# Performance work log

Hardware: AMD Instinct MI355X
Metric: run time of the kernel (lower is better)

The kernel has to match this reference:

```python
import jax, jax.numpy as jnp
import numpy as np

B, T, D_IN, D_H, D_CODE, N_CODES, D_OUT = 64, 512, 1024, 512, 256, 128, 100


def setup_inputs() -> dict:
    key = jax.random.key(0)
    ks = jax.random.split(key, 8)
    x = jax.random.normal(ks[0], (B, T, D_IN), dtype=jnp.float32)
    W1 = jax.random.normal(ks[1], (D_IN, D_H), dtype=jnp.float32) * (1.0 / np.sqrt(D_IN))
    b1 = jnp.zeros((D_H,), jnp.float32)
    W2 = jax.random.normal(ks[2], (D_H, D_CODE), dtype=jnp.float32) * (1.0 / np.sqrt(D_H))
    b2 = jnp.zeros((D_CODE,), jnp.float32)
    codebook = jax.random.normal(ks[3], (N_CODES, D_CODE), dtype=jnp.float32)
    Wd = jax.random.normal(ks[4], (D_CODE, D_OUT), dtype=jnp.float32) * (1.0 / np.sqrt(D_CODE))
    bd = jnp.zeros((D_OUT,), jnp.float32)
    return {"x": x, "W1": W1, "b1": b1, "W2": W2, "b2": b2,
            "codebook": codebook, "Wd": Wd, "bd": bd}


def reference(x, W1, b1, W2, b2, codebook, Wd, bd):
    Bb, Tt, _ = x.shape
    # Encoder (per-timestep loop in torch == one batched matmul)
    h = jax.nn.relu(jnp.einsum('btd,dh->bth', x, W1) + b1)
    encoded = jnp.einsum('bth,hc->btc', h, W2) + b2          # [B,T,256]
    flat = encoded.reshape(-1, D_CODE)                        # [B*T,256]
    # Squared euclidean distances (argmin identical to cdist argmin)
    d2 = (jnp.sum(flat * flat, axis=1, keepdims=True)
          - 2.0 * flat @ codebook.T
          + jnp.sum(codebook * codebook, axis=1))             # [B*T,128]
    token_indices = jnp.argmin(d2, axis=-1)                   # [B*T]
    quantized = codebook[token_indices].reshape(Bb, Tt, D_CODE)
    commitment_loss = jnp.mean((encoded - jax.lax.stop_gradient(quantized)) ** 2)
    codebook_loss = jnp.mean((quantized - jax.lax.stop_gradient(encoded)) ** 2)
    # decoded is computed in the torch model but never returned (dead code)
    pooled = encoded.mean(axis=1)
    decoded = pooled @ Wd + bd  # noqa: F841 (pruned by XLA, kept for fidelity)
    total_loss = commitment_loss + 0.25 * codebook_loss
    return (token_indices.reshape(Bb, Tt), commitment_loss, codebook_loss, total_loss)
```

## Files before the change

### kernel.cpp

```cpp
#include <hip/hip_runtime.h>
#include <cstddef>
#include <cstdint>

static constexpr int M_ROWS  = 32768;
static constexpr int D_INK   = 1024;
static constexpr int D_HID   = 512;
static constexpr int D_CODE_ = 256;
static constexpr int N_CODES_= 128;

static constexpr float TAU_GAP = 0.20f;

using f16x8 = __attribute__((ext_vector_type(8))) _Float16;
using f32x4 = __attribute__((ext_vector_type(4))) float;


__device__ __forceinline__ void dma16(const void* g, void* l) {
    __builtin_amdgcn_global_load_lds(
        (const __attribute__((address_space(1))) void*)g,
        (__attribute__((address_space(3))) void*)l, 16, 0, 0);
}

__device__ __forceinline__ void stage_panel(const _Float16* __restrict__ p,
                                            _Float16* dst, int w, int lane)
{
    #pragma unroll
    for (int ii = 0; ii < 2; ++ii) {
        const int I = 2 * w + ii;
        dma16(p + (size_t)I * 512 + lane * 8, dst + (size_t)I * 512);
    }
}

__device__ __forceinline__ void mfma_tile(const _Float16* sA, const _Float16* sB,
                                          int wm, int wn, int kq, int lm,
                                          f32x4 (&acc)[4][4])
{
    f16x8 a[4];
    #pragma unroll
    for (int fm = 0; fm < 4; ++fm)
        a[fm] = *(const f16x8*)(sA + (kq * 128 + wm * 64 + fm * 16 + lm) * 8);
    #pragma unroll
    for (int fn = 0; fn < 4; ++fn) {
        const f16x8 b = *(const f16x8*)(sB + (kq * 128 + wn * 64 + fn * 16 + lm) * 8);
        #pragma unroll
        for (int fm = 0; fm < 4; ++fm)
            acc[fm][fn] = __builtin_amdgcn_mfma_f32_16x16x32_f16(a[fm], b, acc[fm][fn], 0, 0, 0);
    }
}

__device__ __forceinline__ int xcd_swz(int bid, int nwg) {
    const int q = nwg >> 3;
    return (bid & 7) * q + (bid >> 3);
}

__global__ __launch_bounds__(256)
void prep_cb_kernel(const float* __restrict__ cb, _Float16* __restrict__ cbP,
                    float* __restrict__ cbnorm, float* __restrict__ accum,
                    int* __restrict__ cnt)
{
    const int j = blockIdx.x;
    const int t = threadIdx.x;
    const float v = cb[j * D_CODE_ + t];
    const int ks = t >> 5, kq = (t >> 3) & 3, jj = t & 7;
    cbP[((size_t)ks * 512 + kq * 128 + j) * 8 + jj] = (_Float16)v;

    __shared__ float sr[256];
    sr[t] = v * v;
    __syncthreads();
    for (int s = 128; s >= 1; s >>= 1) {
        if (t < s) sr[t] += sr[t + s];
        __syncthreads();
    }
    if (t == 0) cbnorm[j] = sr[0];
    if (j == 0 && t < 2) accum[t] = 0.0f;
    if (j == 0 && t == 2) *cnt = 0;
}

__global__ __launch_bounds__(256)
void pack_w_kernel(const float* __restrict__ W, _Float16* __restrict__ WP,
                   int Kd, int Nd)
{
    const int ks = blockIdx.x, nt = blockIdx.y;
    const int t = threadIdx.x;
    _Float16* dst = WP + ((size_t)nt * (Kd >> 5) + ks) * 4096;
    #pragma unroll
    for (int half = 0; half < 2; ++half) {
        const int f = half * 256 + t;
        const int nc = f & 127, kq = f >> 7;
        f16x8 v;
        #pragma unroll
        for (int j = 0; j < 8; ++j)
            v[j] = (_Float16)W[(size_t)(ks * 32 + kq * 8 + j) * Nd + nt * 128 + nc];
        *(f16x8*)(dst + (size_t)f * 8) = v;
    }
}

__global__ __launch_bounds__(256)
void pack_x_kernel(const float* __restrict__ X, _Float16* __restrict__ XP)
{
    __shared__ _Float16 sh[128][136];
    const int t  = threadIdx.x;
    const int mt = blockIdx.x;
    const int kc = blockIdx.y;

    const float* src = X + (size_t)mt * 128 * D_INK + kc * 128;
    #pragma unroll
    for (int i = 0; i < 16; ++i) {
        const int idx = i * 256 + t;
        const int row = idx >> 5, c4 = idx & 31;
        const float4 v = *(const float4*)(src + (size_t)row * D_INK + c4 * 4);
        _Float16* d = &sh[row][c4 * 4];
        d[0] = (_Float16)v.x; d[1] = (_Float16)v.y;
        d[2] = (_Float16)v.z; d[3] = (_Float16)v.w;
    }
    __syncthreads();

    _Float16* dst = XP + ((size_t)mt * 32 + kc * 4) * 4096;
    #pragma unroll
    for (int s = 0; s < 4; ++s) {
        #pragma unroll
        for (int half = 0; half < 2; ++half) {
            const int f = half * 256 + t;
            const int rc = f & 127, kq = f >> 7;
            const f16x8 v = *(const f16x8*)(&sh[rc][s * 32 + kq * 8]);
            *(f16x8*)(dst + (size_t)s * 4096 + (size_t)f * 8) = v;
        }
    }
}

__global__ __launch_bounds__(256, 4)
void gemm1_kernel(const _Float16* __restrict__ AP, const _Float16* __restrict__ BP,
                  const float* __restrict__ bias, _Float16* __restrict__ CP)
{
    __shared__ _Float16 lds[2][2][4096];

    const int tid  = threadIdx.x;
    const int lane = tid & 63;
    const int w    = tid >> 6;
    const int wm = w >> 1, wn = w & 1;
    const int kq = lane >> 4, lm = lane & 15;

    const int swz = xcd_swz(blockIdx.x, (M_ROWS / 128) * (D_HID / 128));
    const int n0 = (swz & 3) * 128;
    const int m0 = (swz >> 2) * 128;

    const _Float16* Apan = AP + ((size_t)(m0 >> 7) * 32) * 4096;
    const _Float16* Bpan = BP + ((size_t)(n0 >> 7) * 32) * 4096;

    f32x4 acc[4][4] = {};

    stage_panel(Apan, &lds[0][0][0], w, lane);
    stage_panel(Bpan, &lds[0][1][0], w, lane);

    constexpr int NSTEP = D_INK / 32;
    for (int t = 0; t < NSTEP; ++t) {
        const int cur = t & 1, nxt = cur ^ 1;
        __syncthreads();
        if (t + 1 < NSTEP) {
            stage_panel(Apan + (size_t)(t + 1) * 4096, &lds[nxt][0][0], w, lane);
            stage_panel(Bpan + (size_t)(t + 1) * 4096, &lds[nxt][1][0], w, lane);
        }
        mfma_tile(&lds[cur][0][0], &lds[cur][1][0], wm, wn, kq, lm, acc);
    }

    #pragma unroll
    for (int fn = 0; fn < 4; ++fn) {
        const int col = n0 + wn * 64 + fn * 16 + lm;
        const float bv = bias[col];
        #pragma unroll
        for (int fm = 0; fm < 4; ++fm) {
            #pragma unroll
            for (int r = 0; r < 4; ++r) {
                const int row = m0 + wm * 64 + fm * 16 + kq * 4 + r;
                const float v = fmaxf(acc[fm][fn][r] + bv, 0.0f);
                CP[(((size_t)(row >> 7) * 16 + (col >> 5)) * 512
                    + (size_t)((col >> 3) & 3) * 128 + (row & 127)) * 8 + (col & 7)]
                    = (_Float16)v;
            }
        }
    }
}

__global__ __launch_bounds__(256, 4)
void gemm2_kernel(const _Float16* __restrict__ AP, const _Float16* __restrict__ BP,
                  const float* __restrict__ bias, _Float16* __restrict__ CP,
                  float* __restrict__ accum)
{
    __shared__ _Float16 lds[2][2][4096];

    const int tid  = threadIdx.x;
    const int lane = tid & 63;
    const int w    = tid >> 6;
    const int wm = w >> 1, wn = w & 1;
    const int kq = lane >> 4, lm = lane & 15;

    const int swz = xcd_swz(blockIdx.x, (M_ROWS / 128) * (D_CODE_ / 128));
    const int n0 = (swz & 1) * 128;
    const int m0 = (swz >> 1) * 128;

    const _Float16* Apan = AP + ((size_t)(m0 >> 7) * 16) * 4096;
    const _Float16* Bpan = BP + ((size_t)(n0 >> 7) * 16) * 4096;

    f32x4 acc[4][4] = {};

    stage_panel(Apan, &lds[0][0][0], w, lane);
    stage_panel(Bpan, &lds[0][1][0], w, lane);

    constexpr int NSTEP = D_HID / 32;
    for (int t = 0; t < NSTEP; ++t) {
        const int cur = t & 1, nxt = cur ^ 1;
        __syncthreads();
        if (t + 1 < NSTEP) {
            stage_panel(Apan + (size_t)(t + 1) * 4096, &lds[nxt][0][0], w, lane);
            stage_panel(Bpan + (size_t)(t + 1) * 4096, &lds[nxt][1][0], w, lane);
        }
        mfma_tile(&lds[cur][0][0], &lds[cur][1][0], wm, wn, kq, lm, acc);
    }

    float sumsq = 0.0f;
    #pragma unroll
    for (int fn = 0; fn < 4; ++fn) {
        const int col = n0 + wn * 64 + fn * 16 + lm;
        const float bv = bias[col];
        #pragma unroll
        for (int fm = 0; fm < 4; ++fm) {
            #pragma unroll
            for (int r = 0; r < 4; ++r) {
                const int row = m0 + wm * 64 + fm * 16 + kq * 4 + r;
                const float v = acc[fm][fn][r] + bv;
                sumsq = fmaf(v, v, sumsq);
                CP[(((size_t)(row >> 7) * 8 + (col >> 5)) * 512
                    + (size_t)((col >> 3) & 3) * 128 + (row & 127)) * 8 + (col & 7)]
                    = (_Float16)v;
            }
        }
    }
    #pragma unroll
    for (int mk = 1; mk <= 32; mk <<= 1) sumsq += __shfl_xor(sumsq, mk);
    if (lane == 0) atomicAdd(&accum[1], sumsq);
}

__global__ __launch_bounds__(256, 4)
void dist_kernel(const _Float16* __restrict__ AP, const _Float16* __restrict__ BP,
                 const float* __restrict__ cbn,
                 float* __restrict__ outIdx, float* __restrict__ accum,
                 int* __restrict__ cnt, int* __restrict__ list)
{
    __shared__ _Float16 lds[2][2][4096];

    const int tid  = threadIdx.x;
    const int lane = tid & 63;
    const int w    = tid >> 6;
    const int wm = w >> 1, wn = w & 1;
    const int kq = lane >> 4, lm = lane & 15;
    const int m0 = blockIdx.x * 128;

    float cbn_l[4];
    #pragma unroll
    for (int fn = 0; fn < 4; ++fn) cbn_l[fn] = cbn[wn * 64 + fn * 16 + lm];

    const _Float16* Apan = AP + ((size_t)(m0 >> 7) * 8) * 4096;

    f32x4 acc[4][4] = {};

    stage_panel(Apan, &lds[0][0][0], w, lane);
    stage_panel(BP,   &lds[0][1][0], w, lane);

    constexpr int NSTEP = D_CODE_ / 32;
    for (int t = 0; t < NSTEP; ++t) {
        const int cur = t & 1, nxt = cur ^ 1;
        __syncthreads();
        if (t + 1 < NSTEP) {
            stage_panel(Apan + (size_t)(t + 1) * 4096, &lds[nxt][0][0], w, lane);
            stage_panel(BP   + (size_t)(t + 1) * 4096, &lds[nxt][1][0], w, lane);
        }
        mfma_tile(&lds[cur][0][0], &lds[cur][1][0], wm, wn, kq, lm, acc);
    }

    __syncthreads();
    float* eb1 = (float*)&lds[0][0][0];
    float* eb2 = eb1 + 256;
    int*   eix = (int*)(eb2 + 256);

    #pragma unroll
    for (int fm = 0; fm < 4; ++fm) {
        #pragma unroll
        for (int r = 0; r < 4; ++r) {
            float b1v = 3.4e38f, b2v = 3.4e38f; int bi = 0;
            #pragma unroll
            for (int fn = 0; fn < 4; ++fn) {
                const float v = fmaf(-2.0f, acc[fm][fn][r], cbn_l[fn]);
                if (v < b1v) { b2v = b1v; b1v = v; bi = wn * 64 + fn * 16 + lm; }
                else if (v < b2v) b2v = v;
            }
            #pragma unroll
            for (int mk = 1; mk <= 8; mk <<= 1) {
                const float o1 = __shfl_xor(b1v, mk);
                const float o2 = __shfl_xor(b2v, mk);
                const int   oi = __shfl_xor(bi,  mk);
                if (o1 < b1v || (o1 == b1v && oi < bi)) { b2v = fminf(b1v, o2); b1v = o1; bi = oi; }
                else b2v = fminf(b2v, o1);
            }
            const int rl = wm * 64 + fm * 16 + kq * 4 + r;
            if (lm == 0) { eb1[wn * 128 + rl] = b1v; eb2[wn * 128 + rl] = b2v; eix[wn * 128 + rl] = bi; }
        }
    }
    __syncthreads();

    if (tid < 128) {
        const int rl = tid;
        const float a1 = eb1[rl], a2 = eb2[rl]; const int ai = eix[rl];
        const float o1 = eb1[128 + rl], o2 = eb2[128 + rl]; const int oi = eix[128 + rl];
        float B1, B2; int BI;
        if (o1 < a1 || (o1 == a1 && oi < ai)) { B1 = o1; BI = oi; B2 = fminf(a1, o2); }
        else                                  { B1 = a1; BI = ai; B2 = fminf(a2, o1); }
        outIdx[m0 + rl] = (float)BI;
        if (B2 - B1 < TAU_GAP) { const int p = atomicAdd(cnt, 1); list[p] = m0 + rl; }
        float s = B1;
        #pragma unroll
        for (int mk = 1; mk <= 32; mk <<= 1) s += __shfl_xor(s, mk);
        if (lane == 0) atomicAdd(&accum[0], s);
    }
}

__global__ __launch_bounds__(256)
void fixup_kernel(const float* __restrict__ x, const float* __restrict__ W1,
                  const float* __restrict__ b1, const float* __restrict__ W2,
                  const float* __restrict__ b2, const float* __restrict__ cb,
                  const float* __restrict__ cbnorm,
                  const int* __restrict__ cnt, const int* __restrict__ list,
                  float* __restrict__ outIdx)
{
    __shared__ float xr[1024];
    __shared__ float hr[512];
    __shared__ float er[256];
    __shared__ float dv[128];
    __shared__ int   di[128];

    const int tid = threadIdx.x;
    const int n = *cnt;
    for (int it = blockIdx.x; it < n; it += gridDim.x) {
        const int row = list[it];
        __syncthreads();
        #pragma unroll
        for (int i = 0; i < 4; ++i)
            xr[tid + i * 256] = x[(size_t)row * D_INK + tid + i * 256];
        __syncthreads();
        {
            const int c = tid * 2;
            float s0a = 0.f, s0b = 0.f, s1a = 0.f, s1b = 0.f;
            #pragma unroll 4
            for (int k = 0; k < D_INK; k += 2) {
                const float xv0 = xr[k], xv1 = xr[k + 1];
                const float2 w0 = *(const float2*)(W1 + (size_t)k * D_HID + c);
                const float2 w1 = *(const float2*)(W1 + (size_t)(k + 1) * D_HID + c);
                s0a = fmaf(xv0, w0.x, s0a); s1a = fmaf(xv0, w0.y, s1a);
                s0b = fmaf(xv1, w1.x, s0b); s1b = fmaf(xv1, w1.y, s1b);
            }
            hr[c]     = fmaxf(s0a + s0b + b1[c], 0.f);
            hr[c + 1] = fmaxf(s1a + s1b + b1[c + 1], 0.f);
        }
        __syncthreads();
        {
            float sa = 0.f, sb = 0.f;
            #pragma unroll 4
            for (int k = 0; k < D_HID; k += 2) {
                sa = fmaf(hr[k],     W2[(size_t)k * D_CODE_ + tid],       sa);
                sb = fmaf(hr[k + 1], W2[(size_t)(k + 1) * D_CODE_ + tid], sb);
            }
            er[tid] = sa + sb + b2[tid];
        }
        __syncthreads();
        if (tid < 128) {
            float e2a = 0.f, e2b = 0.f, da = 0.f, db = 0.f;
            const float* cr = cb + (size_t)tid * D_CODE_;
            #pragma unroll 4
            for (int k = 0; k < D_CODE_; k += 2) {
                e2a = fmaf(er[k], er[k], e2a);         e2b = fmaf(er[k + 1], er[k + 1], e2b);
                da  = fmaf(er[k], cr[k], da);          db  = fmaf(er[k + 1], cr[k + 1], db);
            }
            dv[tid] = ((e2a + e2b) - 2.0f * (da + db)) + cbnorm[tid];
            di[tid] = tid;
        }
        __syncthreads();
        for (int st = 64; st >= 1; st >>= 1) {
            if (tid < st) {
                const float a = dv[tid], b = dv[tid + st];
                const int  ib = di[tid + st];
                if (b < a || (b == a && ib < di[tid])) { dv[tid] = b; di[tid] = ib; }
            }
            __syncthreads();
        }
        if (tid == 0) outIdx[row] = (float)di[0];
    }
}

__global__ void finalize_kernel(const float* __restrict__ accum, float* __restrict__ out)
{
    const float inv = 1.0f / (32768.0f * 256.0f);
    const float loss = (accum[0] + accum[1]) * inv;
    out[32768] = loss;
    out[32769] = loss;
    out[32770] = 1.25f * loss;
}

extern "C" void kernel_launch(void* const* d_in, const int* in_sizes, int n_in,
                              void* d_out, int out_size, void* d_ws, size_t ws_size,
                              hipStream_t stream)
{
    (void)in_sizes; (void)n_in; (void)out_size; (void)ws_size;

    const float* x  = (const float*)d_in[0];
    const float* W1 = (const float*)d_in[1];
    const float* b1 = (const float*)d_in[2];
    const float* W2 = (const float*)d_in[3];
    const float* b2 = (const float*)d_in[4];
    const float* cb = (const float*)d_in[5];
    float* out = (float*)d_out;

    char* ws = (char*)d_ws;
    _Float16* W1P  = (_Float16*)(ws + 0);
    _Float16* W2P  = (_Float16*)(ws + 1048576);
    _Float16* cbP  = (_Float16*)(ws + 1310720);
    float*    cbn  = (float*   )(ws + 1376256);
    float*    accum= (float*   )(ws + 1376768);
    int*      cnt  = (int*     )(ws + 1376832);
    int*      list = (int*     )(ws + 1376896);
    _Float16* xP   = (_Float16*)(ws + (size_t)(2u<<20));
    _Float16* encP = (_Float16*)(ws + (size_t)(2u<<20));
    _Float16* hP   = (_Float16*)(ws + (size_t)(2u<<20) + 67108864);

    prep_cb_kernel<<<N_CODES_, 256, 0, stream>>>(cb, cbP, cbn, accum, cnt);
    pack_w_kernel<<<dim3(D_INK / 32, D_HID / 128), 256, 0, stream>>>(W1, W1P, D_INK, D_HID);
    pack_w_kernel<<<dim3(D_HID / 32, D_CODE_ / 128), 256, 0, stream>>>(W2, W2P, D_HID, D_CODE_);
    pack_x_kernel<<<dim3(M_ROWS / 128, D_INK / 128), 256, 0, stream>>>(x, xP);

    gemm1_kernel<<<(M_ROWS / 128) * (D_HID / 128), 256, 0, stream>>>(xP, W1P, b1, hP);
    gemm2_kernel<<<(M_ROWS / 128) * (D_CODE_ / 128), 256, 0, stream>>>(hP, W2P, b2, encP, accum);
    dist_kernel<<<M_ROWS / 128, 256, 0, stream>>>(encP, cbP, cbn, out, accum, cnt, list);
    fixup_kernel<<<512, 256, 0, stream>>>(x, W1, b1, W2, b2, cb, cbn, cnt, list, out);
    finalize_kernel<<<1, 1, 0, stream>>>(accum, out);
}
```

Measured before the change: 288.5 us.

## Batch fixup rows eight per block to reuse weight loads across rows

The fp32 fixup kernel now handles eight ambiguous rows per block iteration, so each W1, W2 and codebook element read from global memory is reused for eight rows instead of one. The codebook is also stored transposed so the distance step reads it coalesced. The grid shrinks to 256 blocks and shared memory grows to about 60KB, which costs occupancy and parallelism when few rows are flagged. The first argmin step drops the equal-value index tie-break, which can change tie behaviour.

```diff
diff --git a/kernel.cpp b/kernel.cpp
--- a/kernel.cpp
+++ b/kernel.cpp
@@ -54,6 +54,7 @@
 
 __global__ __launch_bounds__(256)
 void prep_cb_kernel(const float* __restrict__ cb, _Float16* __restrict__ cbP,
+                    float* __restrict__ cbT,
                     float* __restrict__ cbnorm, float* __restrict__ accum,
                     int* __restrict__ cnt)
 {
@@ -62,6 +63,7 @@
     const float v = cb[j * D_CODE_ + t];
     const int ks = t >> 5, kq = (t >> 3) & 3, jj = t & 7;
     cbP[((size_t)ks * 512 + kq * 128 + j) * 8 + jj] = (_Float16)v;
+    cbT[(size_t)t * N_CODES_ + j] = v;
 
     __shared__ float sr[256];
     sr[t] = v * v;
@@ -325,72 +327,115 @@
 __global__ __launch_bounds__(256)
 void fixup_kernel(const float* __restrict__ x, const float* __restrict__ W1,
                   const float* __restrict__ b1, const float* __restrict__ W2,
-                  const float* __restrict__ b2, const float* __restrict__ cb,
+                  const float* __restrict__ b2, const float* __restrict__ cbT,
                   const float* __restrict__ cbnorm,
                   const int* __restrict__ cnt, const int* __restrict__ list,
                   float* __restrict__ outIdx)
 {
-    __shared__ float xr[1024];
-    __shared__ float hr[512];
-    __shared__ float er[256];
-    __shared__ float dv[128];
-    __shared__ int   di[128];
+    __shared__ float xr[8][1024];
+    __shared__ float hr[8][512];
+    __shared__ float er[8][256];
+    __shared__ float dv[8][128];
+    __shared__ int   di[8][128];
 
     const int tid = threadIdx.x;
     const int n = *cnt;
-    for (int it = blockIdx.x; it < n; it += gridDim.x) {
-        const int row = list[it];
-        __syncthreads();
-        #pragma unroll
-        for (int i = 0; i < 4; ++i)
-            xr[tid + i * 256] = x[(size_t)row * D_INK + tid + i * 256];
-        __syncthreads();
+    const int ngroups = (n + 7) >> 3;
+
+    for (int g = blockIdx.x; g < ngroups; g += gridDim.x) {
+        const int base = g * 8;
+        const int nr = n - base < 8 ? n - base : 8;
+        __syncthreads();
+        #pragma unroll
+        for (int r = 0; r < 8; ++r) {
+            if (r < nr) {
+                const int row = list[base + r];
+                *(float4*)&xr[r][tid * 4] =
+                    *(const float4*)(x + (size_t)row * D_INK + tid * 4);
+            }
+        }
+        __syncthreads();
+
         {
             const int c = tid * 2;
-            float s0a = 0.f, s0b = 0.f, s1a = 0.f, s1b = 0.f;
-            #pragma unroll 4
-            for (int k = 0; k < D_INK; k += 2) {
-                const float xv0 = xr[k], xv1 = xr[k + 1];
-                const float2 w0 = *(const float2*)(W1 + (size_t)k * D_HID + c);
-                const float2 w1 = *(const float2*)(W1 + (size_t)(k + 1) * D_HID + c);
-                s0a = fmaf(xv0, w0.x, s0a); s1a = fmaf(xv0, w0.y, s1a);
-                s0b = fmaf(xv1, w1.x, s0b); s1b = fmaf(xv1, w1.y, s1b);
-            }
-            hr[c]     = fmaxf(s0a + s0b + b1[c], 0.f);
-            hr[c + 1] = fmaxf(s1a + s1b + b1[c + 1], 0.f);
-        }
-        __syncthreads();
+            float a0[8], a1[8];
+            #pragma unroll
+            for (int r = 0; r < 8; ++r) { a0[r] = 0.f; a1[r] = 0.f; }
+            for (int k = 0; k < D_INK; ++k) {
+                const float2 wv = *(const float2*)(W1 + (size_t)k * D_HID + c);
+                #pragma unroll
+                for (int r = 0; r < 8; ++r) {
+                    const float xv = xr[r][k];
+                    a0[r] = fmaf(xv, wv.x, a0[r]);
+                    a1[r] = fmaf(xv, wv.y, a1[r]);
+                }
+            }
+            #pragma unroll
+            for (int r = 0; r < 8; ++r) {
+                hr[r][c]     = fmaxf(a0[r] + b1[c], 0.f);
+                hr[r][c + 1] = fmaxf(a1[r] + b1[c + 1], 0.f);
+            }
+        }
+        __syncthreads();
+
         {
-            float sa = 0.f, sb = 0.f;
-            #pragma unroll 4
-            for (int k = 0; k < D_HID; k += 2) {
-                sa = fmaf(hr[k],     W2[(size_t)k * D_CODE_ + tid],       sa);
-                sb = fmaf(hr[k + 1], W2[(size_t)(k + 1) * D_CODE_ + tid], sb);
-            }
-            er[tid] = sa + sb + b2[tid];
-        }
-        __syncthreads();
-        if (tid < 128) {
-            float e2a = 0.f, e2b = 0.f, da = 0.f, db = 0.f;
-            const float* cr = cb + (size_t)tid * D_CODE_;
-            #pragma unroll 4
-            for (int k = 0; k < D_CODE_; k += 2) {
-                e2a = fmaf(er[k], er[k], e2a);         e2b = fmaf(er[k + 1], er[k + 1], e2b);
-                da  = fmaf(er[k], cr[k], da);          db  = fmaf(er[k + 1], cr[k + 1], db);
-            }
-            dv[tid] = ((e2a + e2b) - 2.0f * (da + db)) + cbnorm[tid];
-            di[tid] = tid;
-        }
-        __syncthreads();
-        for (int st = 64; st >= 1; st >>= 1) {
-            if (tid < st) {
-                const float a = dv[tid], b = dv[tid + st];
-                const int  ib = di[tid + st];
-                if (b < a || (b == a && ib < di[tid])) { dv[tid] = b; di[tid] = ib; }
+            float a[8];
+            #pragma unroll
+            for (int r = 0; r < 8; ++r) a[r] = 0.f;
+            for (int k = 0; k < D_HID; ++k) {
+                const float wv = W2[(size_t)k * D_CODE_ + tid];
+                #pragma unroll
+                for (int r = 0; r < 8; ++r)
+                    a[r] = fmaf(hr[r][k], wv, a[r]);
+            }
+            #pragma unroll
+            for (int r = 0; r < 8; ++r)
+                er[r][tid] = a[r] + b2[tid];
+        }
+        __syncthreads();
+
+        {
+            const int j = tid & 127, half = tid >> 7;
+            float e2[4], dt[4];
+            #pragma unroll
+            for (int q = 0; q < 4; ++q) { e2[q] = 0.f; dt[q] = 0.f; }
+            for (int k = 0; k < D_CODE_; ++k) {
+                const float cv = cbT[(size_t)k * N_CODES_ + j];
+                #pragma unroll
+                for (int q = 0; q < 4; ++q) {
+                    const float ev = er[half * 4 + q][k];
+                    e2[q] = fmaf(ev, ev, e2[q]);
+                    dt[q] = fmaf(ev, cv, dt[q]);
+                }
+            }
+            #pragma unroll
+            for (int q = 0; q < 4; ++q) {
+                dv[half * 4 + q][j] = (e2[q] - 2.0f * dt[q]) + cbnorm[j];
+                di[half * 4 + q][j] = j;
+            }
+        }
+        __syncthreads();
+
+        #pragma unroll
+        for (int pass = 0; pass < 2; ++pass) {
+            const int r = pass * 4 + (tid >> 6);
+            const int i = tid & 63;
+            {
+                const float a = dv[r][i], b = dv[r][i + 64];
+                const int  ib = di[r][i + 64];
+                if (b < a) { dv[r][i] = b; di[r][i] = ib; }
             }
             __syncthreads();
-        }
-        if (tid == 0) outIdx[row] = (float)di[0];
+            for (int st = 32; st >= 1; st >>= 1) {
+                if (i < st) {
+                    const float a = dv[r][i], b = dv[r][i + st];
+                    const int  ib = di[r][i + st];
+                    if (b < a || (b == a && ib < di[r][i])) { dv[r][i] = b; di[r][i] = ib; }
+                }
+                __syncthreads();
+            }
+        }
+        if (tid < nr) outIdx[list[base + tid]] = (float)di[tid][0];
     }
 }
 
@@ -425,11 +470,12 @@
     float*    accum= (float*   )(ws + 1376768);
     int*      cnt  = (int*     )(ws + 1376832);
     int*      list = (int*     )(ws + 1376896);
+    float*    cbT  = (float*   )(ws + 1507968);
     _Float16* xP   = (_Float16*)(ws + (size_t)(2u<<20));
     _Float16* encP = (_Float16*)(ws + (size_t)(2u<<20));
     _Float16* hP   = (_Float16*)(ws + (size_t)(2u<<20) + 67108864);
 
-    prep_cb_kernel<<<N_CODES_, 256, 0, stream>>>(cb, cbP, cbn, accum, cnt);
+    prep_cb_kernel<<<N_CODES_, 256, 0, stream>>>(cb, cbP, cbT, cbn, accum, cnt);
     pack_w_kernel<<<dim3(D_INK / 32, D_HID / 128), 256, 0, stream>>>(W1, W1P, D_INK, D_HID);
     pack_w_kernel<<<dim3(D_HID / 32, D_CODE_ / 128), 256, 0, stream>>>(W2, W2P, D_HID, D_CODE_);
     pack_x_kernel<<<dim3(M_ROWS / 128, D_INK / 128), 256, 0, stream>>>(x, xP);
@@ -437,6 +483,6 @@
     gemm1_kernel<<<(M_ROWS / 128) * (D_HID / 128), 256, 0, stream>>>(xP, W1P, b1, hP);
     gemm2_kernel<<<(M_ROWS / 128) * (D_CODE_ / 128), 256, 0, stream>>>(hP, W2P, b2, encP, accum);
     dist_kernel<<<M_ROWS / 128, 256, 0, stream>>>(encP, cbP, cbn, out, accum, cnt, list);
-    fixup_kernel<<<512, 256, 0, stream>>>(x, W1, b1, W2, b2, cb, cbn, cnt, list, out);
+    fixup_kernel<<<256, 256, 0, stream>>>(x, W1, b1, W2, b2, cbT, cbn, cnt, list, out);
     finalize_kernel<<<1, 1, 0, stream>>>(accum, out);
 }
```

Measured after the change: 268.6 us. 1.07x faster.
